# Optimization experiments

Hardware: AMD Instinct MI355X
Metric: run time of the kernel (lower is better)

Reference implementation:

```python
import jax, jax.numpy as jnp
import numpy as np

B, S, R, C_M = 1, 512, 256, 256   # batch, n_seq, n_res, msa channels
C_P, C_Z = 32, 128                # projection channels, pair channels


def setup_inputs() -> dict:
    key = jax.random.key(0)
    ks = jax.random.split(key, 8)
    M = jax.random.normal(ks[0], (B, S, R, C_M), dtype=jnp.float32)
    M_mask = jnp.ones((B, S, R), dtype=jnp.float32)
    Z_raw = jnp.zeros((B, R, R, C_Z), dtype=jnp.float32)
    # LayerNorm params
    ln_g = jnp.ones((C_M,), dtype=jnp.float32)
    ln_b = jnp.zeros((C_M,), dtype=jnp.float32)
    # linear_a / linear_b: glorot-uniform init
    lim = float(np.sqrt(6.0 / (C_M + C_P)))
    Wa = jax.random.uniform(ks[1], (C_P, C_M), minval=-lim, maxval=lim, dtype=jnp.float32)
    ba = jnp.zeros((C_P,), dtype=jnp.float32)
    Wb = jax.random.uniform(ks[2], (C_P, C_M), minval=-lim, maxval=lim, dtype=jnp.float32)
    bb = jnp.zeros((C_P,), dtype=jnp.float32)
    # o_linear is zero-initialized in the source; use small random weights so the
    # output is non-trivial for correctness testing (math is identical).
    Wo = jax.random.normal(ks[3], (C_Z, C_P * C_P), dtype=jnp.float32) * 0.02
    bo = jnp.zeros((C_Z,), dtype=jnp.float32)
    return {"M": M, "M_mask": M_mask, "Z_raw": Z_raw, "ln_g": ln_g, "ln_b": ln_b,
            "Wa": Wa, "ba": ba, "Wb": Wb, "bb": bb, "Wo": Wo, "bo": bo}


def _layernorm(x, g, b, eps=1e-5):
    mu = jnp.mean(x, axis=-1, keepdims=True)
    var = jnp.var(x, axis=-1, keepdims=True)
    return (x - mu) * jax.lax.rsqrt(var + eps) * g + b


def reference(M, M_mask, Z_raw, ln_g, ln_b, Wa, ba, Wb, bb, Wo, bo):
    Mn = _layernorm(M, ln_g, ln_b)                      # [b,s,i,c_m]
    mask = M_mask[..., None]                            # [b,s,i,1]
    left = (jnp.einsum('bsic,dc->bsid', Mn, Wa) + ba) * mask   # [b,s,i,d]
    right = (jnp.einsum('bsic,ec->bsie', Mn, Wb) + bb) * mask  # [b,s,j,e]
    # outer-product mean: contract over sequence dim s
    O = jnp.einsum('bsid,bsje->bijde', left, right)     # [b,i,j,d,e]
    b, i, j, d, e = O.shape
    O = O.reshape(b, i, j, d * e)
    Z = jnp.einsum('bijk,zk->bijz', O, Wo) + bo         # [b,i,j,c_z]
    norm = jnp.einsum('bsi,bsj->bij', M_mask, M_mask)[..., None]
    return Z / (1e-3 + norm)
```

## Files before the change

### kernel.cpp

```cpp
#include <hip/hip_runtime.h>
#include <hip/hip_bf16.h>
#include <stdint.h>

#define S_DIM 512
#define R_DIM 256
#define CM 256
#define CP 32
#define CZ 128

typedef __attribute__((ext_vector_type(8))) short bf16x8;
typedef __attribute__((ext_vector_type(4))) float f32x4;
typedef unsigned int u32;

__device__ __forceinline__ float bf2f(unsigned short u) {
  union { u32 i; float f; } v; v.i = ((u32)u) << 16; return v.f;
}
__device__ __forceinline__ unsigned short f2bf(float f) {
  union { float f; u32 i; } v; v.f = f;
  u32 x = v.i;
  u32 r = (x + 0x7FFFu + ((x >> 16) & 1u)) >> 16;
  return (unsigned short)r;
}

__device__ __forceinline__ void gload_lds16(const unsigned short* g, unsigned short* l) {
  __builtin_amdgcn_global_load_lds((const __attribute__((address_space(1))) u32*)(g),
                                   (__attribute__((address_space(3))) u32*)(l), 16, 0, 0);
}

__device__ __forceinline__ void wave_bar() {
  asm volatile("" ::: "memory");
  __builtin_amdgcn_s_barrier();
  asm volatile("" ::: "memory");
}

__global__ __launch_bounds__(256) void
fused_prep_kernel(const float* __restrict__ Wa, const float* __restrict__ ba,
                  const float* __restrict__ Wb, const float* __restrict__ bb,
                  const float* __restrict__ ln_g, const float* __restrict__ ln_b,
                  const float* __restrict__ Wo, const float* __restrict__ mask,
                  unsigned short* __restrict__ wp, float* __restrict__ Ka,
                  float* __restrict__ Ca, unsigned short* __restrict__ Wo_bf,
                  float* __restrict__ scale) {
  const int b = blockIdx.x;
  const int t = threadIdx.x;
  if (b < 64) {
    __shared__ float ska[4], sca[4];
    const int o = b;
    const float* W = (o < 32) ? (Wa + o * CM) : (Wb + (o - 32) * CM);
    float wv = W[t];
    unsigned short bv = f2bf(wv * ln_g[t]);
    wp[o * CM + t] = bv;
    float ka = bf2f(bv);
    float ca = wv * ln_b[t];
    #pragma unroll
    for (int m = 1; m < 64; m <<= 1) {
      ka += __shfl_xor(ka, m);
      ca += __shfl_xor(ca, m);
    }
    if ((t & 63) == 0) { ska[t >> 6] = ka; sca[t >> 6] = ca; }
    __syncthreads();
    if (t == 0) {
      Ka[o] = ska[0] + ska[1] + ska[2] + ska[3];
      Ca[o] = sca[0] + sca[1] + sca[2] + sca[3] + ((o < 32) ? ba[o] : bb[o - 32]);
    }
  } else if (b < 576) {
    int idx = (b - 64) * 256 + t;
    int z = idx >> 10, k = idx & 1023;
    int d = k >> 5, e = k & 31;
    Wo_bf[(z << 10) + e * 32 + d] = f2bf(Wo[idx]);
  } else {
    const int i = b - 576, j = t;
    float sum = 0.f;
    for (int s = 0; s < S_DIM; ++s)
      sum += mask[s * R_DIM + i] * mask[s * R_DIM + j];
    scale[i * R_DIM + j] = 1.0f / (1e-3f + sum);
  }
}

#define K1_ROWS 64
#define XPAD 264

__global__ __launch_bounds__(256) void
ln_proj_kernel(const float* __restrict__ M, const float* __restrict__ mask,
               const unsigned short* __restrict__ wp_g, const float* __restrict__ Ka_g,
               const float* __restrict__ Ca_g,
               unsigned short* __restrict__ leftT, unsigned short* __restrict__ rightT) {
  __shared__ unsigned short xt[K1_ROWS * XPAD];
  __shared__ unsigned short wp[64 * XPAD];
  __shared__ float smu[K1_ROWS], srs[K1_ROWS], smk[K1_ROWS];
  __shared__ float sKa[64], sCa[64];

  const int t = threadIdx.x;
  const int lane = t & 63;
  const int w = t >> 6;
  const int lm = lane & 15;
  const int rr = lane >> 4;
  const int i = blockIdx.x;
  const int s0 = blockIdx.y * K1_ROWS;

  for (int idx = t; idx < 64 * CM / 8; idx += 256) {
    int row = idx >> 5;
    int col = (idx & 31) * 8;
    *(uint4*)(&wp[row * XPAD + col]) = *(const uint4*)(wp_g + row * CM + col);
  }
  if (t < 64) { sKa[t] = Ka_g[t]; sCa[t] = Ca_g[t]; }

  #pragma unroll
  for (int it = 0; it < 4; ++it) {
    const int row = w * 16 + it * 4 + rr;
    const int sg = s0 + row;
    const float* src = M + ((size_t)sg * R_DIM + i) * CM;
    float4 x[4];
    #pragma unroll
    for (int ch = 0; ch < 4; ++ch) x[ch] = *(const float4*)(src + ch * 64 + lm * 4);
    float sum = 0.f, ssq = 0.f;
    #pragma unroll
    for (int ch = 0; ch < 4; ++ch) {
      sum += x[ch].x + x[ch].y + x[ch].z + x[ch].w;
      ssq += x[ch].x * x[ch].x + x[ch].y * x[ch].y + x[ch].z * x[ch].z + x[ch].w * x[ch].w;
    }
    #pragma unroll
    for (int m = 1; m < 16; m <<= 1) {
      sum += __shfl_xor(sum, m);
      ssq += __shfl_xor(ssq, m);
    }
    float mu = sum * (1.0f / CM);
    float var = ssq * (1.0f / CM) - mu * mu;
    float rs = rsqrtf(var + 1e-5f);
    if (lm == 0) {
      smu[row] = mu; srs[row] = rs;
      smk[row] = mask[(size_t)sg * R_DIM + i];
    }
    #pragma unroll
    for (int ch = 0; ch < 4; ++ch) {
      ushort4 xb;
      xb.x = f2bf(x[ch].x); xb.y = f2bf(x[ch].y); xb.z = f2bf(x[ch].z); xb.w = f2bf(x[ch].w);
      *(ushort4*)(&xt[row * XPAD + ch * 64 + lm * 4]) = xb;
    }
  }
  __syncthreads();

  f32x4 acc[4] = {{0.f, 0.f, 0.f, 0.f}, {0.f, 0.f, 0.f, 0.f},
                  {0.f, 0.f, 0.f, 0.f}, {0.f, 0.f, 0.f, 0.f}};
  #pragma unroll
  for (int k = 0; k < 8; ++k) {
    const int c0 = k * 32 + ((lane >> 4) << 3);
    bf16x8 a = *(const bf16x8*)(&wp[(w * 16 + (lane & 15)) * XPAD + c0]);
    #pragma unroll
    for (int nt = 0; nt < 4; ++nt) {
      bf16x8 b = *(const bf16x8*)(&xt[(nt * 16 + (lane & 15)) * XPAD + c0]);
      acc[nt] = __builtin_amdgcn_mfma_f32_16x16x32_bf16(a, b, acc[nt], 0, 0, 0);
    }
  }

  #pragma unroll
  for (int nt = 0; nt < 4; ++nt) {
    int srow = nt * 16 + (lane & 15);
    float mu = smu[srow], rs = srs[srow], mk = smk[srow];
    int sg = s0 + srow;
    #pragma unroll
    for (int r = 0; r < 4; ++r) {
      int o = w * 16 + ((lane >> 4) << 2) + r;
      float v = (rs * (acc[nt][r] - mu * sKa[o]) + sCa[o]) * mk;
      unsigned short bv = f2bf(v);
      if (o < 32) leftT[(size_t)(i * 32 + o) * S_DIM + sg] = bv;
      else        rightT[(size_t)(i * 32 + (o - 32)) * S_DIM + sg] = bv;
    }
  }
}

#define NT2 8

__global__ __launch_bounds__(1024) void
opm_gemm_kernel(const unsigned short* __restrict__ leftT, const unsigned short* __restrict__ rightT,
                const unsigned short* __restrict__ Wo_bf, const float* __restrict__ bo,
                const float* __restrict__ scale, float* __restrict__ out) {
  extern __shared__ unsigned short smem[];

  const int t = threadIdx.x;
  const int lane = t & 63;
  const int lm = lane & 15, lq = lane >> 4;
  const int sw = lm & 7;
  const int w = t >> 6;
  const int wmm = w >> 2, wnn = w & 3;

  const int bid = blockIdx.x;
  const int xcd = bid & 7, local = bid >> 3;
  const int by = xcd * 4 + (local & 3);
  const int bx = local >> 2;

  const unsigned short* Asrc = leftT + (size_t)(by * 256) * S_DIM;
  const unsigned short* Bsrc = rightT + (size_t)(bx * 256) * S_DIM;

  int sr[2], so[2];
  #pragma unroll
  for (int q = 0; q < 2; ++q) {
    int c = q * 1024 + t;
    sr[q] = c >> 3;
    so[q] = ((c & 7) ^ ((c >> 3) & 7)) * 8;
  }

  f32x4 acc[4][4];
  #pragma unroll
  for (int a = 0; a < 4; ++a)
    #pragma unroll
    for (int b = 0; b < 4; ++b) acc[a][b] = (f32x4){0.f, 0.f, 0.f, 0.f};

  auto STAGE = [&](int kt, int buf) {
    const int kb = kt * 64;
    unsigned short* ab = smem + buf * 32768;
    #pragma unroll
    for (int q = 0; q < 2; ++q) {
      int c = q * 1024 + t;
      gload_lds16(Asrc + (size_t)sr[q] * S_DIM + kb + so[q], ab + c * 8);
      gload_lds16(Bsrc + (size_t)sr[q] * S_DIM + kb + so[q], ab + 16384 + c * 8);
    }
  };

  STAGE(0, 0);
  STAGE(1, 1);

  #pragma unroll
  for (int kt = 0; kt < NT2; ++kt) {
    const int cur = kt & 1;
    if (kt < NT2 - 1) asm volatile("s_waitcnt vmcnt(4)" ::: "memory");
    else              asm volatile("s_waitcnt vmcnt(0)" ::: "memory");
    wave_bar();

    const unsigned short* Ab = smem + cur * 32768;
    const unsigned short* Bb = Ab + 16384;
    #pragma unroll
    for (int ks = 0; ks < 2; ++ks) {
      const int kp = ks * 4 + lq;
      const int slot = (kp ^ sw) << 3;
      bf16x8 af[4], bfr[4];
      #pragma unroll
      for (int mi = 0; mi < 4; ++mi)
        af[mi] = *(const bf16x8*)(&Ab[(wmm * 64 + mi * 16 + lm) * 64 + slot]);
      #pragma unroll
      for (int ni = 0; ni < 4; ++ni)
        bfr[ni] = *(const bf16x8*)(&Bb[(wnn * 64 + ni * 16 + lm) * 64 + slot]);
      __builtin_amdgcn_s_setprio(1);
      #pragma unroll
      for (int mi = 0; mi < 4; ++mi)
        #pragma unroll
        for (int ni = 0; ni < 4; ++ni)
          acc[mi][ni] = __builtin_amdgcn_mfma_f32_16x16x32_bf16(af[mi], bfr[ni], acc[mi][ni], 0, 0, 0);
      __builtin_amdgcn_s_setprio(0);
    }

    wave_bar();
    if (kt + 2 < NT2) STAGE(kt + 2, cur);
  }

  #pragma unroll
  for (int mi = 0; mi < 4; ++mi) {
    const int m0 = wmm * 64 + mi * 16 + lq * 4;
    const int il = m0 >> 5, d0 = m0 & 31;
    #pragma unroll
    for (int ni = 0; ni < 4; ++ni) {
      const int n = wnn * 64 + ni * 16 + lm;
      const int jl = n >> 5, e = n & 31;
      const int pair = il * 8 + jl;
      u32 off = ((u32)(64 * e + 2 * d0)) ^ ((u32)(e & 7) << 4) ^ ((u32)(pair & 7) << 4);
      ushort4 v4;
      v4.x = f2bf(acc[mi][ni][0]); v4.y = f2bf(acc[mi][ni][1]);
      v4.z = f2bf(acc[mi][ni][2]); v4.w = f2bf(acc[mi][ni][3]);
      *(ushort4*)((char*)smem + (u32)pair * 2048 + off) = v4;
    }
  }
  __syncthreads();

  const int wz = w & 7, wph = w >> 3;
  f32x4 zacc[2] = {{0.f, 0.f, 0.f, 0.f}, {0.f, 0.f, 0.f, 0.f}};
  const unsigned short* wsrc = Wo_bf + (size_t)(wz * 16 + lm) * (CP * CP) + lq * 8;
  #pragma unroll 8
  for (int kk = 0; kk < 32; ++kk) {
    bf16x8 bw = *(const bf16x8*)(wsrc + kk * 32);
    #pragma unroll
    for (int pt = 0; pt < 2; ++pt) {
      const int pairL = wph * 32 + pt * 16 + lm;
      u32 off = ((u32)(kk * 64 + lq * 16)) ^ ((u32)(kk & 7) << 4) ^ ((u32)(pairL & 7) << 4);
      bf16x8 a = *(const bf16x8*)((const char*)smem + (u32)pairL * 2048 + off);
      zacc[pt] = __builtin_amdgcn_mfma_f32_16x16x32_bf16(a, bw, zacc[pt], 0, 0, 0);
    }
  }

  const int z = wz * 16 + lm;
  const float bz = bo[z];
  #pragma unroll
  for (int pt = 0; pt < 2; ++pt) {
    #pragma unroll
    for (int r = 0; r < 4; ++r) {
      const int pair = wph * 32 + pt * 16 + lq * 4 + r;
      const int ig = by * 8 + (pair >> 3), jg = bx * 8 + (pair & 7);
      float v = (zacc[pt][r] + bz) * scale[ig * R_DIM + jg];
      out[((size_t)ig * R_DIM + jg) * CZ + z] = v;
    }
  }
}

extern "C" void kernel_launch(void* const* d_in, const int* in_sizes, int n_in,
                              void* d_out, int out_size, void* d_ws, size_t ws_size,
                              hipStream_t stream) {
  const float* M     = (const float*)d_in[0];
  const float* Mmask = (const float*)d_in[1];
  const float* ln_g  = (const float*)d_in[3];
  const float* ln_b  = (const float*)d_in[4];
  const float* Wa    = (const float*)d_in[5];
  const float* ba    = (const float*)d_in[6];
  const float* Wb    = (const float*)d_in[7];
  const float* bb    = (const float*)d_in[8];
  const float* Wo    = (const float*)d_in[9];
  const float* bo    = (const float*)d_in[10];
  float* out = (float*)d_out;

  char* ws = (char*)d_ws;
  unsigned short* leftT  = (unsigned short*)(ws);
  unsigned short* rightT = (unsigned short*)(ws + 8388608);
  unsigned short* wp     = (unsigned short*)(ws + 16777216);
  float*          Ka     = (float*)(ws + 16810240);
  float*          Ca     = (float*)(ws + 16810496);
  unsigned short* Wo_bf  = (unsigned short*)(ws + 16810752);
  float*          scale  = (float*)(ws + 17072896);
  (void)ws_size; (void)in_sizes; (void)n_in; (void)out_size;

  hipFuncSetAttribute((const void*)opm_gemm_kernel,
                      hipFuncAttributeMaxDynamicSharedMemorySize, 131072);

  hipLaunchKernelGGL(fused_prep_kernel, dim3(832), dim3(256), 0, stream,
                     Wa, ba, Wb, bb, ln_g, ln_b, Wo, Mmask, wp, Ka, Ca, Wo_bf, scale);
  hipLaunchKernelGGL(ln_proj_kernel, dim3(R_DIM, S_DIM / K1_ROWS), dim3(256), 0, stream,
                     M, Mmask, wp, Ka, Ca, leftT, rightT);
  hipLaunchKernelGGL(opm_gemm_kernel, dim3(1024), dim3(1024), 131072, stream,
                     leftT, rightT, Wo_bf, bo, scale, out);
}
```

Baseline: 184.7 us.

## Restructure OPM GEMM to 512 threads with triple-buffered ping-pong K pipeline

The OPM GEMM block shrinks from 16 to 8 waves. Each wave now computes a 128x64 tile (8x4 MFMA accumulators), so fragment reuse per LDS read is higher. The K loop is rebuilt around three 32-wide K stages in LDS with split half-tile MFMA phases, interleaving barriers, loads and compute in a ping-pong schedule. The Wo epilogue is redistributed over 8 waves with 4 pair tiles each. The goal is to overlap global-to-LDS loads with MFMA work and cut LDS traffic, at the cost of more registers, more barriers and lower wave count per CU.

```diff
diff --git a/kernel.cpp b/kernel.cpp
--- a/kernel.cpp
+++ b/kernel.cpp
@@ -25,12 +25,6 @@
 __device__ __forceinline__ void gload_lds16(const unsigned short* g, unsigned short* l) {
   __builtin_amdgcn_global_load_lds((const __attribute__((address_space(1))) u32*)(g),
                                    (__attribute__((address_space(3))) u32*)(l), 16, 0, 0);
-}
-
-__device__ __forceinline__ void wave_bar() {
-  asm volatile("" ::: "memory");
-  __builtin_amdgcn_s_barrier();
-  asm volatile("" ::: "memory");
 }
 
 __global__ __launch_bounds__(256) void
@@ -171,7 +165,7 @@
 
 #define NT2 8
 
-__global__ __launch_bounds__(1024) void
+__global__ __launch_bounds__(512, 1) void
 opm_gemm_kernel(const unsigned short* __restrict__ leftT, const unsigned short* __restrict__ rightT,
                 const unsigned short* __restrict__ Wo_bf, const float* __restrict__ bo,
                 const float* __restrict__ scale, float* __restrict__ out) {
@@ -180,9 +174,8 @@
   const int t = threadIdx.x;
   const int lane = t & 63;
   const int lm = lane & 15, lq = lane >> 4;
-  const int sw = lm & 7;
   const int w = t >> 6;
-  const int wmm = w >> 2, wnn = w & 3;
+  const int wm = w >> 2, wn = w & 3;
 
   const int bid = blockIdx.x;
   const int xcd = bid & 7, local = bid >> 3;
@@ -192,74 +185,126 @@
   const unsigned short* Asrc = leftT + (size_t)(by * 256) * S_DIM;
   const unsigned short* Bsrc = rightT + (size_t)(bx * 256) * S_DIM;
 
-  int sr[2], so[2];
+  int srow[2], ssrc[2], sdst[2];
   #pragma unroll
   for (int q = 0; q < 2; ++q) {
-    int c = q * 1024 + t;
-    sr[q] = c >> 3;
-    so[q] = ((c & 7) ^ ((c >> 3) & 7)) * 8;
-  }
-
-  f32x4 acc[4][4];
-  #pragma unroll
-  for (int a = 0; a < 4; ++a)
+    int c = q * 512 + t;
+    int row = c >> 2, sl = c & 3;
+    srow[q] = row;
+    ssrc[q] = (sl ^ ((row >> 1) & 3)) * 8;
+    sdst[q] = row * 32 + sl * 8;
+  }
+
+  f32x4 acc[8][4];
+  #pragma unroll
+  for (int a = 0; a < 8; ++a)
     #pragma unroll
     for (int b = 0; b < 4; ++b) acc[a][b] = (f32x4){0.f, 0.f, 0.f, 0.f};
 
-  auto STAGE = [&](int kt, int buf) {
-    const int kb = kt * 64;
-    unsigned short* ab = smem + buf * 32768;
+  auto STAGE = [&](int s) {
+    unsigned short* base = smem + (s % 3) * 16384;
+    const int kb = s * 32;
     #pragma unroll
     for (int q = 0; q < 2; ++q) {
-      int c = q * 1024 + t;
-      gload_lds16(Asrc + (size_t)sr[q] * S_DIM + kb + so[q], ab + c * 8);
-      gload_lds16(Bsrc + (size_t)sr[q] * S_DIM + kb + so[q], ab + 16384 + c * 8);
+      gload_lds16(Asrc + (size_t)srow[q] * S_DIM + kb + ssrc[q], base + sdst[q]);
+      gload_lds16(Bsrc + (size_t)srow[q] * S_DIM + kb + ssrc[q], base + 8192 + sdst[q]);
     }
   };
 
-  STAGE(0, 0);
-  STAGE(1, 1);
+  const int sl8 = (lq ^ ((lm >> 1) & 3)) * 8;
+
+  bf16x8 afl[4], afh[4], bfr[4];
+
+  STAGE(0); STAGE(1);
+  asm volatile("s_waitcnt vmcnt(4)" ::: "memory");
+  __builtin_amdgcn_s_barrier();
 
   #pragma unroll
   for (int kt = 0; kt < NT2; ++kt) {
-    const int cur = kt & 1;
-    if (kt < NT2 - 1) asm volatile("s_waitcnt vmcnt(4)" ::: "memory");
-    else              asm volatile("s_waitcnt vmcnt(0)" ::: "memory");
-    wave_bar();
-
-    const unsigned short* Ab = smem + cur * 32768;
-    const unsigned short* Bb = Ab + 16384;
-    #pragma unroll
-    for (int ks = 0; ks < 2; ++ks) {
-      const int kp = ks * 4 + lq;
-      const int slot = (kp ^ sw) << 3;
-      bf16x8 af[4], bfr[4];
-      #pragma unroll
-      for (int mi = 0; mi < 4; ++mi)
-        af[mi] = *(const bf16x8*)(&Ab[(wmm * 64 + mi * 16 + lm) * 64 + slot]);
+    const unsigned short* A0 = smem + ((2 * kt) % 3) * 16384;
+    const unsigned short* B0 = A0 + 8192;
+    const unsigned short* A1 = smem + ((2 * kt + 1) % 3) * 16384;
+    const unsigned short* B1 = A1 + 8192;
+
+    if (kt + 1 < NT2) STAGE(2 * kt + 2);
+    #pragma unroll
+    for (int mi = 0; mi < 4; ++mi)
+      afl[mi] = *(const bf16x8*)(&A0[(wm * 128 + mi * 16 + lm) * 32 + sl8]);
+    #pragma unroll
+    for (int ni = 0; ni < 4; ++ni)
+      bfr[ni] = *(const bf16x8*)(&B0[(wn * 64 + ni * 16 + lm) * 32 + sl8]);
+    __builtin_amdgcn_s_barrier();
+    asm volatile("s_waitcnt lgkmcnt(0)" ::: "memory");
+    __builtin_amdgcn_sched_barrier(0);
+    __builtin_amdgcn_s_setprio(1);
+    #pragma unroll
+    for (int mi = 0; mi < 4; ++mi)
       #pragma unroll
       for (int ni = 0; ni < 4; ++ni)
-        bfr[ni] = *(const bf16x8*)(&Bb[(wnn * 64 + ni * 16 + lm) * 64 + slot]);
-      __builtin_amdgcn_s_setprio(1);
+        acc[mi][ni] = __builtin_amdgcn_mfma_f32_16x16x32_bf16(afl[mi], bfr[ni], acc[mi][ni], 0, 0, 0);
+    __builtin_amdgcn_s_setprio(0);
+    __builtin_amdgcn_s_barrier();
+
+    #pragma unroll
+    for (int mi = 0; mi < 4; ++mi)
+      afh[mi] = *(const bf16x8*)(&A0[(wm * 128 + (4 + mi) * 16 + lm) * 32 + sl8]);
+    __builtin_amdgcn_s_barrier();
+    asm volatile("s_waitcnt lgkmcnt(0)" ::: "memory");
+    __builtin_amdgcn_sched_barrier(0);
+    __builtin_amdgcn_s_setprio(1);
+    #pragma unroll
+    for (int mi = 0; mi < 4; ++mi)
       #pragma unroll
-      for (int mi = 0; mi < 4; ++mi)
-        #pragma unroll
-        for (int ni = 0; ni < 4; ++ni)
-          acc[mi][ni] = __builtin_amdgcn_mfma_f32_16x16x32_bf16(af[mi], bfr[ni], acc[mi][ni], 0, 0, 0);
-      __builtin_amdgcn_s_setprio(0);
-    }
-
-    wave_bar();
-    if (kt + 2 < NT2) STAGE(kt + 2, cur);
-  }
-
-  #pragma unroll
-  for (int mi = 0; mi < 4; ++mi) {
-    const int m0 = wmm * 64 + mi * 16 + lq * 4;
+      for (int ni = 0; ni < 4; ++ni)
+        acc[4 + mi][ni] = __builtin_amdgcn_mfma_f32_16x16x32_bf16(afh[mi], bfr[ni], acc[4 + mi][ni], 0, 0, 0);
+    __builtin_amdgcn_s_setprio(0);
+    if (kt == NT2 - 1) asm volatile("s_waitcnt vmcnt(0)" ::: "memory");
+    else               asm volatile("s_waitcnt vmcnt(4)" ::: "memory");
+    __builtin_amdgcn_s_barrier();
+
+    if (kt + 1 < NT2) STAGE(2 * kt + 3);
+    #pragma unroll
+    for (int mi = 0; mi < 4; ++mi)
+      afl[mi] = *(const bf16x8*)(&A1[(wm * 128 + mi * 16 + lm) * 32 + sl8]);
+    #pragma unroll
+    for (int ni = 0; ni < 4; ++ni)
+      bfr[ni] = *(const bf16x8*)(&B1[(wn * 64 + ni * 16 + lm) * 32 + sl8]);
+    __builtin_amdgcn_s_barrier();
+    asm volatile("s_waitcnt lgkmcnt(0)" ::: "memory");
+    __builtin_amdgcn_sched_barrier(0);
+    __builtin_amdgcn_s_setprio(1);
+    #pragma unroll
+    for (int mi = 0; mi < 4; ++mi)
+      #pragma unroll
+      for (int ni = 0; ni < 4; ++ni)
+        acc[mi][ni] = __builtin_amdgcn_mfma_f32_16x16x32_bf16(afl[mi], bfr[ni], acc[mi][ni], 0, 0, 0);
+    __builtin_amdgcn_s_setprio(0);
+    __builtin_amdgcn_s_barrier();
+
+    #pragma unroll
+    for (int mi = 0; mi < 4; ++mi)
+      afh[mi] = *(const bf16x8*)(&A1[(wm * 128 + (4 + mi) * 16 + lm) * 32 + sl8]);
+    __builtin_amdgcn_s_barrier();
+    asm volatile("s_waitcnt lgkmcnt(0)" ::: "memory");
+    __builtin_amdgcn_sched_barrier(0);
+    __builtin_amdgcn_s_setprio(1);
+    #pragma unroll
+    for (int mi = 0; mi < 4; ++mi)
+      #pragma unroll
+      for (int ni = 0; ni < 4; ++ni)
+        acc[4 + mi][ni] = __builtin_amdgcn_mfma_f32_16x16x32_bf16(afh[mi], bfr[ni], acc[4 + mi][ni], 0, 0, 0);
+    __builtin_amdgcn_s_setprio(0);
+    if (kt + 1 < NT2) asm volatile("s_waitcnt vmcnt(4)" ::: "memory");
+    __builtin_amdgcn_s_barrier();
+  }
+
+  #pragma unroll
+  for (int mi = 0; mi < 8; ++mi) {
+    const int m0 = wm * 128 + mi * 16 + lq * 4;
     const int il = m0 >> 5, d0 = m0 & 31;
     #pragma unroll
     for (int ni = 0; ni < 4; ++ni) {
-      const int n = wnn * 64 + ni * 16 + lm;
+      const int n = wn * 64 + ni * 16 + lm;
       const int jl = n >> 5, e = n & 31;
       const int pair = il * 8 + jl;
       u32 off = ((u32)(64 * e + 2 * d0)) ^ ((u32)(e & 7) << 4) ^ ((u32)(pair & 7) << 4);
@@ -271,28 +316,28 @@
   }
   __syncthreads();
 
-  const int wz = w & 7, wph = w >> 3;
-  f32x4 zacc[2] = {{0.f, 0.f, 0.f, 0.f}, {0.f, 0.f, 0.f, 0.f}};
-  const unsigned short* wsrc = Wo_bf + (size_t)(wz * 16 + lm) * (CP * CP) + lq * 8;
-  #pragma unroll 8
+  f32x4 zacc[4] = {{0.f, 0.f, 0.f, 0.f}, {0.f, 0.f, 0.f, 0.f},
+                   {0.f, 0.f, 0.f, 0.f}, {0.f, 0.f, 0.f, 0.f}};
+  const unsigned short* wsrc = Wo_bf + (size_t)(w * 16 + lm) * (CP * CP) + lq * 8;
+  #pragma unroll 4
   for (int kk = 0; kk < 32; ++kk) {
     bf16x8 bw = *(const bf16x8*)(wsrc + kk * 32);
     #pragma unroll
-    for (int pt = 0; pt < 2; ++pt) {
-      const int pairL = wph * 32 + pt * 16 + lm;
+    for (int pt = 0; pt < 4; ++pt) {
+      const int pairL = pt * 16 + lm;
       u32 off = ((u32)(kk * 64 + lq * 16)) ^ ((u32)(kk & 7) << 4) ^ ((u32)(pairL & 7) << 4);
       bf16x8 a = *(const bf16x8*)((const char*)smem + (u32)pairL * 2048 + off);
       zacc[pt] = __builtin_amdgcn_mfma_f32_16x16x32_bf16(a, bw, zacc[pt], 0, 0, 0);
     }
   }
 
-  const int z = wz * 16 + lm;
+  const int z = w * 16 + lm;
   const float bz = bo[z];
   #pragma unroll
-  for (int pt = 0; pt < 2; ++pt) {
+  for (int pt = 0; pt < 4; ++pt) {
     #pragma unroll
     for (int r = 0; r < 4; ++r) {
-      const int pair = wph * 32 + pt * 16 + lq * 4 + r;
+      const int pair = pt * 16 + lq * 4 + r;
       const int ig = by * 8 + (pair >> 3), jg = bx * 8 + (pair & 7);
       float v = (zacc[pt][r] + bz) * scale[ig * R_DIM + jg];
       out[((size_t)ig * R_DIM + jg) * CZ + z] = v;
@@ -332,6 +377,6 @@
                      Wa, ba, Wb, bb, ln_g, ln_b, Wo, Mmask, wp, Ka, Ca, Wo_bf, scale);
   hipLaunchKernelGGL(ln_proj_kernel, dim3(R_DIM, S_DIM / K1_ROWS), dim3(256), 0, stream,
                      M, Mmask, wp, Ka, Ca, leftT, rightT);
-  hipLaunchKernelGGL(opm_gemm_kernel, dim3(1024), dim3(1024), 131072, stream,
+  hipLaunchKernelGGL(opm_gemm_kernel, dim3(1024), dim3(512), 131072, stream,
                      leftT, rightT, Wo_bf, bo, scale, out);
 }
```

Result: faster. 162.3 us (-12.1%).

## Rework OPM GEMM to 32x32x16 MFMA with 512 threads and k-major LDS layout

Applied to the files above, without the earlier changes.

Switches the outer-product GEMM and the Wo projection from 16x16x32 to 32x32x16 bf16 MFMA tiles. The block shrinks from 1024 to 512 threads, so each wave owns a 128x64 tile. The staging layout becomes k-chunk-major instead of an XOR-swizzled row layout, and the intermediate pair buffer uses a new swizzle. The intent is fewer LDS fragment reads per FLOP and higher MFMA efficiency. The cost is higher register pressure, half as many waves for latency hiding, and a dropped s_setprio and outer-loop unroll.

```diff
diff --git a/kernel.cpp b/kernel.cpp
--- a/kernel.cpp
+++ b/kernel.cpp
@@ -10,6 +10,7 @@
 
 typedef __attribute__((ext_vector_type(8))) short bf16x8;
 typedef __attribute__((ext_vector_type(4))) float f32x4;
+typedef __attribute__((ext_vector_type(16))) float f32x16;
 typedef unsigned int u32;
 
 __device__ __forceinline__ float bf2f(unsigned short u) {
@@ -171,7 +172,7 @@
 
 #define NT2 8
 
-__global__ __launch_bounds__(1024) void
+__global__ __launch_bounds__(512, 1) void
 opm_gemm_kernel(const unsigned short* __restrict__ leftT, const unsigned short* __restrict__ rightT,
                 const unsigned short* __restrict__ Wo_bf, const float* __restrict__ bo,
                 const float* __restrict__ scale, float* __restrict__ out) {
@@ -179,10 +180,9 @@
 
   const int t = threadIdx.x;
   const int lane = t & 63;
-  const int lm = lane & 15, lq = lane >> 4;
-  const int sw = lm & 7;
+  const int l31 = lane & 31, lq2 = lane >> 5;
   const int w = t >> 6;
-  const int wmm = w >> 2, wnn = w & 3;
+  const int wm = w >> 2, wn = w & 3;
 
   const int bid = blockIdx.x;
   const int xcd = bid & 7, local = bid >> 3;
@@ -192,111 +192,106 @@
   const unsigned short* Asrc = leftT + (size_t)(by * 256) * S_DIM;
   const unsigned short* Bsrc = rightT + (size_t)(bx * 256) * S_DIM;
 
-  int sr[2], so[2];
-  #pragma unroll
-  for (int q = 0; q < 2; ++q) {
-    int c = q * 1024 + t;
-    sr[q] = c >> 3;
-    so[q] = ((c & 7) ^ ((c >> 3) & 7)) * 8;
-  }
-
-  f32x4 acc[4][4];
+  int aoff[4], ldso[4];
+  #pragma unroll
+  for (int q = 0; q < 4; ++q) {
+    int c = q * 512 + t;
+    aoff[q] = (c & 255) * S_DIM + (c >> 8) * 8;
+    ldso[q] = c * 8;
+  }
+
+  f32x16 acc[4][2];
   #pragma unroll
   for (int a = 0; a < 4; ++a)
     #pragma unroll
-    for (int b = 0; b < 4; ++b) acc[a][b] = (f32x4){0.f, 0.f, 0.f, 0.f};
+    for (int b = 0; b < 2; ++b)
+      #pragma unroll
+      for (int r = 0; r < 16; ++r) acc[a][b][r] = 0.f;
 
   auto STAGE = [&](int kt, int buf) {
     const int kb = kt * 64;
     unsigned short* ab = smem + buf * 32768;
     #pragma unroll
-    for (int q = 0; q < 2; ++q) {
-      int c = q * 1024 + t;
-      gload_lds16(Asrc + (size_t)sr[q] * S_DIM + kb + so[q], ab + c * 8);
-      gload_lds16(Bsrc + (size_t)sr[q] * S_DIM + kb + so[q], ab + 16384 + c * 8);
+    for (int q = 0; q < 4; ++q) {
+      gload_lds16(Asrc + aoff[q] + kb, ab + ldso[q]);
+      gload_lds16(Bsrc + aoff[q] + kb, ab + 16384 + ldso[q]);
     }
   };
 
   STAGE(0, 0);
   STAGE(1, 1);
 
-  #pragma unroll
+  int arow[4], brow[2];
+  #pragma unroll
+  for (int mi = 0; mi < 4; ++mi) arow[mi] = (wm * 128 + mi * 32 + l31) * 8;
+  #pragma unroll
+  for (int ni = 0; ni < 2; ++ni) brow[ni] = 16384 + (wn * 64 + ni * 32 + l31) * 8;
+
   for (int kt = 0; kt < NT2; ++kt) {
-    const int cur = kt & 1;
-    if (kt < NT2 - 1) asm volatile("s_waitcnt vmcnt(4)" ::: "memory");
+    if (kt < NT2 - 1) asm volatile("s_waitcnt vmcnt(8)" ::: "memory");
     else              asm volatile("s_waitcnt vmcnt(0)" ::: "memory");
     wave_bar();
 
-    const unsigned short* Ab = smem + cur * 32768;
-    const unsigned short* Bb = Ab + 16384;
-    #pragma unroll
-    for (int ks = 0; ks < 2; ++ks) {
-      const int kp = ks * 4 + lq;
-      const int slot = (kp ^ sw) << 3;
-      bf16x8 af[4], bfr[4];
-      #pragma unroll
-      for (int mi = 0; mi < 4; ++mi)
-        af[mi] = *(const bf16x8*)(&Ab[(wmm * 64 + mi * 16 + lm) * 64 + slot]);
-      #pragma unroll
-      for (int ni = 0; ni < 4; ++ni)
-        bfr[ni] = *(const bf16x8*)(&Bb[(wnn * 64 + ni * 16 + lm) * 64 + slot]);
-      __builtin_amdgcn_s_setprio(1);
+    const unsigned short* Ab = smem + (kt & 1) * 32768;
+    #pragma unroll
+    for (int ks = 0; ks < 4; ++ks) {
+      const int kbase = (ks * 2 + lq2) * 2048;
+      bf16x8 af[4], bf[2];
+      #pragma unroll
+      for (int mi = 0; mi < 4; ++mi) af[mi] = *(const bf16x8*)(Ab + kbase + arow[mi]);
+      #pragma unroll
+      for (int ni = 0; ni < 2; ++ni) bf[ni] = *(const bf16x8*)(Ab + kbase + brow[ni]);
       #pragma unroll
       for (int mi = 0; mi < 4; ++mi)
         #pragma unroll
-        for (int ni = 0; ni < 4; ++ni)
-          acc[mi][ni] = __builtin_amdgcn_mfma_f32_16x16x32_bf16(af[mi], bfr[ni], acc[mi][ni], 0, 0, 0);
-      __builtin_amdgcn_s_setprio(0);
+        for (int ni = 0; ni < 2; ++ni)
+          acc[mi][ni] = __builtin_amdgcn_mfma_f32_32x32x16_bf16(af[mi], bf[ni], acc[mi][ni], 0, 0, 0);
     }
 
     wave_bar();
-    if (kt + 2 < NT2) STAGE(kt + 2, cur);
+    if (kt + 2 < NT2) STAGE(kt + 2, kt & 1);
   }
 
   #pragma unroll
   for (int mi = 0; mi < 4; ++mi) {
-    const int m0 = wmm * 64 + mi * 16 + lq * 4;
-    const int il = m0 >> 5, d0 = m0 & 31;
-    #pragma unroll
-    for (int ni = 0; ni < 4; ++ni) {
-      const int n = wnn * 64 + ni * 16 + lm;
-      const int jl = n >> 5, e = n & 31;
-      const int pair = il * 8 + jl;
-      u32 off = ((u32)(64 * e + 2 * d0)) ^ ((u32)(e & 7) << 4) ^ ((u32)(pair & 7) << 4);
-      ushort4 v4;
-      v4.x = f2bf(acc[mi][ni][0]); v4.y = f2bf(acc[mi][ni][1]);
-      v4.z = f2bf(acc[mi][ni][2]); v4.w = f2bf(acc[mi][ni][3]);
-      *(ushort4*)((char*)smem + (u32)pair * 2048 + off) = v4;
+    #pragma unroll
+    for (int ni = 0; ni < 2; ++ni) {
+      const int pair = (wm * 4 + mi) * 8 + wn * 2 + ni;
+      const u32 pbyte = (u32)((pair ^ l31) * 16 + lq2 * 8);
+      #pragma unroll
+      for (int g = 0; g < 4; ++g) {
+        const u32 byte = (u32)(l31 * 4 + g) * 1024 + pbyte;
+        ushort4 v4;
+        v4.x = f2bf(acc[mi][ni][g * 4 + 0]);
+        v4.y = f2bf(acc[mi][ni][g * 4 + 1]);
+        v4.z = f2bf(acc[mi][ni][g * 4 + 2]);
+        v4.w = f2bf(acc[mi][ni][g * 4 + 3]);
+        *(ushort4*)((char*)smem + byte) = v4;
+      }
     }
   }
   __syncthreads();
 
-  const int wz = w & 7, wph = w >> 3;
-  f32x4 zacc[2] = {{0.f, 0.f, 0.f, 0.f}, {0.f, 0.f, 0.f, 0.f}};
-  const unsigned short* wsrc = Wo_bf + (size_t)(wz * 16 + lm) * (CP * CP) + lq * 8;
-  #pragma unroll 8
-  for (int kk = 0; kk < 32; ++kk) {
-    bf16x8 bw = *(const bf16x8*)(wsrc + kk * 32);
-    #pragma unroll
-    for (int pt = 0; pt < 2; ++pt) {
-      const int pairL = wph * 32 + pt * 16 + lm;
-      u32 off = ((u32)(kk * 64 + lq * 16)) ^ ((u32)(kk & 7) << 4) ^ ((u32)(pairL & 7) << 4);
-      bf16x8 a = *(const bf16x8*)((const char*)smem + (u32)pairL * 2048 + off);
-      zacc[pt] = __builtin_amdgcn_mfma_f32_16x16x32_bf16(a, bw, zacc[pt], 0, 0, 0);
-    }
-  }
-
-  const int z = wz * 16 + lm;
+  f32x16 zacc;
+  #pragma unroll
+  for (int r = 0; r < 16; ++r) zacc[r] = 0.f;
+  const unsigned short* wop = Wo_bf + (size_t)(wn * 32 + l31) * (CP * CP) + lq2 * 8;
+  #pragma unroll 4
+  for (int kk = 0; kk < 64; ++kk) {
+    bf16x8 bw = *(const bf16x8*)(wop + kk * 16);
+    const u32 ob = (u32)(kk * 2 + lq2) * 1024 + (u32)(((wm * 32 + l31) ^ (kk >> 1)) * 16);
+    bf16x8 oa = *(const bf16x8*)((const char*)smem + ob);
+    zacc = __builtin_amdgcn_mfma_f32_32x32x16_bf16(oa, bw, zacc, 0, 0, 0);
+  }
+
+  const int z = wn * 32 + l31;
   const float bz = bo[z];
   #pragma unroll
-  for (int pt = 0; pt < 2; ++pt) {
-    #pragma unroll
-    for (int r = 0; r < 4; ++r) {
-      const int pair = wph * 32 + pt * 16 + lq * 4 + r;
-      const int ig = by * 8 + (pair >> 3), jg = bx * 8 + (pair & 7);
-      float v = (zacc[pt][r] + bz) * scale[ig * R_DIM + jg];
-      out[((size_t)ig * R_DIM + jg) * CZ + z] = v;
-    }
+  for (int r = 0; r < 16; ++r) {
+    const int pair = wm * 32 + (r & 3) + 8 * (r >> 2) + 4 * lq2;
+    const int ig = by * 8 + (pair >> 3), jg = bx * 8 + (pair & 7);
+    float v = (zacc[r] + bz) * scale[ig * R_DIM + jg];
+    out[((size_t)ig * R_DIM + jg) * CZ + z] = v;
   }
 }
 
@@ -332,6 +327,6 @@
                      Wa, ba, Wb, bb, ln_g, ln_b, Wo, Mmask, wp, Ka, Ca, Wo_bf, scale);
   hipLaunchKernelGGL(ln_proj_kernel, dim3(R_DIM, S_DIM / K1_ROWS), dim3(256), 0, stream,
                      M, Mmask, wp, Ka, Ca, leftT, rightT);
-  hipLaunchKernelGGL(opm_gemm_kernel, dim3(1024), dim3(1024), 131072, stream,
+  hipLaunchKernelGGL(opm_gemm_kernel, dim3(1024), dim3(512), 131072, stream,
                      leftT, rightT, Wo_bf, bo, scale, out);
 }
```

Measured after the change: 263.8 us. 1.43x slower.
